# Kernel optimization log

Measured on AMD Instinct MI355X. Metric: run time of the kernel, lower is better.

Reference implementation:

```python
import jax, jax.numpy as jnp
import numpy as np

NB, NQ, NLINKS = 524288, 7, 8


def _cross_matrix(v):
    # v: [..., 3] -> skew-symmetric [..., 3, 3]
    z = jnp.zeros_like(v[..., 0])
    v1, v2, v3 = v[..., 0], v[..., 1], v[..., 2]
    return jnp.stack([
        jnp.stack([z, -v3, v2], axis=-1),
        jnp.stack([v3, z, -v1], axis=-1),
        jnp.stack([-v2, v1, z], axis=-1),
    ], axis=-2)


def _rodrigues(w, th):
    # w: [..., 3] axis (not necessarily unit), th: [...] angle -> [..., 3, 3]
    w_hat = _cross_matrix(w)
    n = jnp.linalg.norm(w, axis=-1)
    a = (jnp.sin(n * th) / n)[..., None, None]
    b = ((1.0 - jnp.cos(n * th)) / (n * n))[..., None, None]
    I = jnp.eye(3, dtype=w.dtype)
    return I + a * w_hat + b * (w_hat @ w_hat)


def _rpy_to_R(rpy):
    # rpy: [n, 3] -> [n, 3, 3]; R = Rz(yaw) @ Ry(pitch) @ Rx(roll)
    n = rpy.shape[0]
    ex = jnp.broadcast_to(jnp.array([1.0, 0.0, 0.0], rpy.dtype), (n, 3))
    ey = jnp.broadcast_to(jnp.array([0.0, 1.0, 0.0], rpy.dtype), (n, 3))
    ez = jnp.broadcast_to(jnp.array([0.0, 0.0, 1.0], rpy.dtype), (n, 3))
    Rx = _rodrigues(ex, rpy[:, 0])
    Ry = _rodrigues(ey, rpy[:, 1])
    Rz = _rodrigues(ez, rpy[:, 2])
    return Rz @ (Ry @ Rx)


def _hom(R, t):
    # R: [..., 3, 3], t: [..., 3] -> [..., 4, 4]
    top = jnp.concatenate([R, t[..., None]], axis=-1)
    last = jnp.broadcast_to(jnp.array([0.0, 0.0, 0.0, 1.0], R.dtype), top.shape[:-2] + (1, 4))
    return jnp.concatenate([top, last], axis=-2)


def setup_inputs() -> dict:
    key = jax.random.key(0)
    k1, k2, k3, k4, k5 = jax.random.split(key, 5)
    return {
        "q": jax.random.normal(k1, (NB, NQ), dtype=jnp.float32),
        "joint_xyz": jax.random.normal(k2, (NQ, 3), dtype=jnp.float32),
        "joint_rpy": jax.random.normal(k3, (NQ, 3), dtype=jnp.float32),
        "joint_axis": jax.random.normal(k4, (NQ, 3), dtype=jnp.float32),
        "link_xyz": jax.random.normal(k5, (NLINKS, 3), dtype=jnp.float32),
        "idx": 6,
    }


def reference(q, joint_xyz, joint_rpy, joint_axis, link_xyz, idx):
    nb, nq = q.shape
    # Constant per-joint fixed frames [nq, 4, 4]
    T_joints = _hom(_rpy_to_R(joint_rpy), joint_xyz)
    # Constant per-link frames (rpy = 0 => identity rotation path) [nlinks, 4, 4]
    T_links = _hom(_rpy_to_R(jnp.zeros_like(link_xyz)), link_xyz)
    # Per-(batch, joint) joint rotation via Rodrigues: w [nq,3], th [nb,nq] -> [nb,nq,3,3]
    Rq = _rodrigues(joint_axis[None, :, :], q)
    Tq = _hom(Rq, jnp.zeros(Rq.shape[:-2] + (3,), Rq.dtype))  # [nb, nq, 4, 4]
    # Per-joint local transform: fixed frame @ joint rotation
    T = T_joints[None, :, :, :] @ Tq  # [nb, nq, 4, 4]
    # Sequential chain over joints (nq is small and fixed)
    T_world = T[:, 0]
    for j in range(1, nq):
        T_world = T_world @ T[:, j]
    return T_world @ T_links[idx][None, :, :]  # [nb, 4, 4]
```

## Files before the change

kernel.cpp:

```cpp
#include <hip/hip_runtime.h>

#define FK_NQ 7
#define FK_BLOCK 256


__device__ __forceinline__ void qmul(const float* a, const float* b, float* r)
{
    r[0] = a[0]*b[0] - a[1]*b[1] - a[2]*b[2] - a[3]*b[3];
    r[1] = a[0]*b[1] + a[1]*b[0] + a[2]*b[3] - a[3]*b[2];
    r[2] = a[0]*b[2] - a[1]*b[3] + a[2]*b[0] + a[3]*b[1];
    r[3] = a[0]*b[3] + a[1]*b[2] - a[2]*b[1] + a[3]*b[0];
}

__global__ __launch_bounds__(FK_BLOCK, 8) void fk_fused(
    const float* __restrict__ q,
    const float* __restrict__ joint_xyz,
    const float* __restrict__ joint_rpy,
    const float* __restrict__ joint_axis,
    const float* __restrict__ link_xyz,
    const int*   __restrict__ idxp,
    float* __restrict__ out,
    unsigned nb)
{
    __shared__ float4 c4[22];
    __shared__ float4 so[FK_BLOCK * 5];

    const int tid = threadIdx.x;
    const unsigned bbase = blockIdx.x * FK_BLOCK;
    const unsigned b = bbase + tid;
    const bool valid = (b < nb);

    float th[FK_NQ];
    if (valid) {
        const float* qp = q + b * FK_NQ;
        #pragma unroll
        for (int j = 0; j < FK_NQ; ++j) th[j] = qp[j];
    }

    if (tid < FK_NQ) {
        const int j = tid;
        float rr = joint_rpy[j*3+0], pp = joint_rpy[j*3+1], yy = joint_rpy[j*3+2];
        float sr, cr, sp2, cp2, sy, cy;
        __sincosf(0.5f*rr, &sr, &cr);
        __sincosf(0.5f*pp, &sp2, &cp2);
        __sincosf(0.5f*yy, &sy, &cy);
        float qx[4] = {cr, sr, 0.f, 0.f};
        float qy[4] = {cp2, 0.f, sp2, 0.f};
        float qz[4] = {cy, 0.f, 0.f, sy};
        float tmp[4], qj[4];
        qmul(qy, qx, tmp);
        qmul(qz, tmp, qj);

        float w0 = joint_axis[j*3+0], w1 = joint_axis[j*3+1], w2 = joint_axis[j*3+2];
        float n  = sqrtf(w0*w0 + w1*w1 + w2*w2);
        float ninv = 1.0f/n;
        float qu[4] = {0.f, w0*ninv, w1*ninv, w2*ninv};
        float qjw[4];
        qmul(qj, qu, qjw);

        c4[j*3+0] = make_float4(qj[0],  qj[1],  qj[2],  qj[3]);
        c4[j*3+1] = make_float4(qjw[0], qjw[1], qjw[2], qjw[3]);
        c4[j*3+2] = make_float4(joint_xyz[j*3+0], joint_xyz[j*3+1],
                                joint_xyz[j*3+2], 0.5f*n);
    } else if (tid == FK_NQ) {
        const int ix = idxp[0];
        c4[21] = make_float4(link_xyz[ix*3+0], link_xyz[ix*3+1],
                             link_xyz[ix*3+2], 0.0f);
    }
    __syncthreads();

    if (valid) {
        float4 j0q = c4[0], j0w = c4[1], j0t = c4[2];
        float sv, cv;
        __sincosf(j0t.w * th[0], &sv, &cv);
        float Qw = cv*j0q.x + sv*j0w.x;
        float Qx = cv*j0q.y + sv*j0w.y;
        float Qy = cv*j0q.z + sv*j0w.z;
        float Qz = cv*j0q.w + sv*j0w.w;
        float tx = j0t.x, ty = j0t.y, tz = j0t.z;

        #pragma unroll
        for (int j = 1; j < FK_NQ; ++j) {
            float4 jq = c4[j*3+0], jw = c4[j*3+1], jt = c4[j*3+2];
            float s, c;
            __sincosf(jt.w * th[j], &s, &c);
            float vx = jt.x, vy = jt.y, vz = jt.z;
            float c1x = Qy*vz - Qz*vy;
            float c1y = Qz*vx - Qx*vz;
            float c1z = Qx*vy - Qy*vx;
            float c2x = Qw*c1x + (Qy*c1z - Qz*c1y);
            float c2y = Qw*c1y + (Qz*c1x - Qx*c1z);
            float c2z = Qw*c1z + (Qx*c1y - Qy*c1x);
            tx += vx + 2.0f*c2x;
            ty += vy + 2.0f*c2y;
            tz += vz + 2.0f*c2z;
            float sw = c*jq.x + s*jw.x;
            float sx = c*jq.y + s*jw.y;
            float sy = c*jq.z + s*jw.z;
            float sz = c*jq.w + s*jw.w;
            float nw = Qw*sw - Qx*sx - Qy*sy - Qz*sz;
            float nx = Qw*sx + Qx*sw + Qy*sz - Qz*sy;
            float ny = Qw*sy - Qx*sz + Qy*sw + Qz*sx;
            float nz = Qw*sz + Qx*sy - Qy*sx + Qz*sw;
            Qw = nw; Qx = nx; Qy = ny; Qz = nz;
        }

        float xx = Qx*Qx, yy = Qy*Qy, zz = Qz*Qz;
        float xy = Qx*Qy, xz = Qx*Qz, yz = Qy*Qz;
        float wx = Qw*Qx, wy = Qw*Qy, wz = Qw*Qz;
        float M00 = 1.0f - 2.0f*(yy+zz);
        float M01 = 2.0f*(xy - wz);
        float M02 = 2.0f*(xz + wy);
        float M10 = 2.0f*(xy + wz);
        float M11 = 1.0f - 2.0f*(xx+zz);
        float M12 = 2.0f*(yz - wx);
        float M20 = 2.0f*(xz - wy);
        float M21 = 2.0f*(yz + wx);
        float M22 = 1.0f - 2.0f*(xx+yy);

        float4 lp = c4[21];
        so[tid*5+0] = make_float4(M00, M01, M02, M00*lp.x + M01*lp.y + M02*lp.z + tx);
        so[tid*5+1] = make_float4(M10, M11, M12, M10*lp.x + M11*lp.y + M12*lp.z + ty);
        so[tid*5+2] = make_float4(M20, M21, M22, M20*lp.x + M21*lp.y + M22*lp.z + tz);
        so[tid*5+3] = make_float4(0.0f, 0.0f, 0.0f, 1.0f);
    }
    __syncthreads();

    if (bbase + FK_BLOCK <= nb) {
        float4* o = (float4*)out + (size_t)bbase * 4u;
        #pragma unroll
        for (int k = 0; k < 4; ++k) {
            unsigned w = k*FK_BLOCK + tid;
            o[w] = so[(w >> 2)*5 + (w & 3)];
        }
    } else if (valid) {
        float4* o = (float4*)(out + (size_t)b * 16u);
        #pragma unroll
        for (int r = 0; r < 4; ++r) o[r] = so[tid*5 + r];
    }
}

extern "C" void kernel_launch(void* const* d_in, const int* in_sizes, int n_in,
                              void* d_out, int out_size, void* d_ws, size_t ws_size,
                              hipStream_t stream) {
    const float* q          = (const float*)d_in[0];
    const float* joint_xyz  = (const float*)d_in[1];
    const float* joint_rpy  = (const float*)d_in[2];
    const float* joint_axis = (const float*)d_in[3];
    const float* link_xyz   = (const float*)d_in[4];
    const int*   idxp       = (const int*)d_in[5];
    float* out = (float*)d_out;

    const unsigned nb = (unsigned)(in_sizes[0] / FK_NQ);
    const int grid = (int)((nb + FK_BLOCK - 1) / FK_BLOCK);

    fk_fused<<<grid, FK_BLOCK, 0, stream>>>(q, joint_xyz, joint_rpy, joint_axis,
                                            link_xyz, idxp, out, nb);
}
```

Measured before the change: 17.18 us.

## Convert to persistent grid-stride kernel with prefetched q and double-buffered staging

Caps the grid at a fixed number of blocks, and each block loops over chunks of the batch. Each iteration prefetches the next chunk's joint angles while computing the current one, and staging alternates between two shared buffers. The per-joint constant setup is then paid once per block rather than once per chunk. The cost is fewer resident waves, doubled shared memory and a dropped occupancy hint in the launch bounds, which may reduce latency hiding on this memory-bound kernel.

```diff
diff --git a/kernel.cpp b/kernel.cpp
--- a/kernel.cpp
+++ b/kernel.cpp
@@ -2,6 +2,7 @@
 
 #define FK_NQ 7
 #define FK_BLOCK 256
+#define MAX_GRID 768
 
 
 __device__ __forceinline__ void qmul(const float* a, const float* b, float* r)
@@ -12,7 +13,7 @@
     r[3] = a[0]*b[3] + a[1]*b[2] - a[2]*b[1] + a[3]*b[0];
 }
 
-__global__ __launch_bounds__(FK_BLOCK, 8) void fk_fused(
+__global__ __launch_bounds__(FK_BLOCK) void fk_fused(
     const float* __restrict__ q,
     const float* __restrict__ joint_xyz,
     const float* __restrict__ joint_rpy,
@@ -23,19 +24,10 @@
     unsigned nb)
 {
     __shared__ float4 c4[22];
-    __shared__ float4 so[FK_BLOCK * 5];
+    __shared__ float4 so[2][FK_BLOCK * 5];
 
     const int tid = threadIdx.x;
-    const unsigned bbase = blockIdx.x * FK_BLOCK;
-    const unsigned b = bbase + tid;
-    const bool valid = (b < nb);
-
-    float th[FK_NQ];
-    if (valid) {
-        const float* qp = q + b * FK_NQ;
-        #pragma unroll
-        for (int j = 0; j < FK_NQ; ++j) th[j] = qp[j];
-    }
+    const unsigned nchunks = (nb + FK_BLOCK - 1) / FK_BLOCK;
 
     if (tid < FK_NQ) {
         const int j = tid;
@@ -67,76 +59,115 @@
         c4[21] = make_float4(link_xyz[ix*3+0], link_xyz[ix*3+1],
                              link_xyz[ix*3+2], 0.0f);
     }
+
+    unsigned c = blockIdx.x;
+    float th[FK_NQ];
+    {
+        const unsigned b = c * FK_BLOCK + tid;
+        if (b < nb) {
+            const float* qp = q + (size_t)b * FK_NQ;
+            #pragma unroll
+            for (int j = 0; j < FK_NQ; ++j) th[j] = qp[j];
+        } else {
+            #pragma unroll
+            for (int j = 0; j < FK_NQ; ++j) th[j] = 0.0f;
+        }
+    }
+
     __syncthreads();
 
-    if (valid) {
-        float4 j0q = c4[0], j0w = c4[1], j0t = c4[2];
-        float sv, cv;
-        __sincosf(j0t.w * th[0], &sv, &cv);
-        float Qw = cv*j0q.x + sv*j0w.x;
-        float Qx = cv*j0q.y + sv*j0w.y;
-        float Qy = cv*j0q.z + sv*j0w.z;
-        float Qz = cv*j0q.w + sv*j0w.w;
-        float tx = j0t.x, ty = j0t.y, tz = j0t.z;
+    int buf = 0;
+    const float4 lp = c4[21];
+
+    for (; c < nchunks; c += gridDim.x) {
+        const unsigned cn = c + gridDim.x;
+        float thn[FK_NQ];
+        #pragma unroll
+        for (int j = 0; j < FK_NQ; ++j) thn[j] = 0.0f;
+        if (cn < nchunks) {
+            const unsigned bn = cn * FK_BLOCK + tid;
+            if (bn < nb) {
+                const float* qp = q + (size_t)bn * FK_NQ;
+                #pragma unroll
+                for (int j = 0; j < FK_NQ; ++j) thn[j] = qp[j];
+            }
+        }
+
+        const unsigned bbase = c * FK_BLOCK;
+        const unsigned b = bbase + tid;
+        if (b < nb) {
+            float sv[FK_NQ], cv[FK_NQ];
+            #pragma unroll
+            for (int j = 0; j < FK_NQ; ++j)
+                __sincosf(c4[j*3+2].w * th[j], &sv[j], &cv[j]);
+
+            float4 j0q = c4[0], j0w = c4[1], j0t = c4[2];
+            float Qw = cv[0]*j0q.x + sv[0]*j0w.x;
+            float Qx = cv[0]*j0q.y + sv[0]*j0w.y;
+            float Qy = cv[0]*j0q.z + sv[0]*j0w.z;
+            float Qz = cv[0]*j0q.w + sv[0]*j0w.w;
+            float tx = j0t.x, ty = j0t.y, tz = j0t.z;
+
+            #pragma unroll
+            for (int j = 1; j < FK_NQ; ++j) {
+                float4 jq = c4[j*3+0], jw = c4[j*3+1], jt = c4[j*3+2];
+                float vx = jt.x, vy = jt.y, vz = jt.z;
+                float c1x = Qy*vz - Qz*vy;
+                float c1y = Qz*vx - Qx*vz;
+                float c1z = Qx*vy - Qy*vx;
+                float c2x = Qw*c1x + (Qy*c1z - Qz*c1y);
+                float c2y = Qw*c1y + (Qz*c1x - Qx*c1z);
+                float c2z = Qw*c1z + (Qx*c1y - Qy*c1x);
+                tx += vx + 2.0f*c2x;
+                ty += vy + 2.0f*c2y;
+                tz += vz + 2.0f*c2z;
+                float sw = cv[j]*jq.x + sv[j]*jw.x;
+                float sx = cv[j]*jq.y + sv[j]*jw.y;
+                float sy2 = cv[j]*jq.z + sv[j]*jw.z;
+                float sz = cv[j]*jq.w + sv[j]*jw.w;
+                float nw = Qw*sw - Qx*sx - Qy*sy2 - Qz*sz;
+                float nx = Qw*sx + Qx*sw + Qy*sz - Qz*sy2;
+                float ny = Qw*sy2 - Qx*sz + Qy*sw + Qz*sx;
+                float nz = Qw*sz + Qx*sy2 - Qy*sx + Qz*sw;
+                Qw = nw; Qx = nx; Qy = ny; Qz = nz;
+            }
+
+            float xx = Qx*Qx, yy = Qy*Qy, zz = Qz*Qz;
+            float xy = Qx*Qy, xz = Qx*Qz, yz = Qy*Qz;
+            float wx = Qw*Qx, wy = Qw*Qy, wz = Qw*Qz;
+            float M00 = 1.0f - 2.0f*(yy+zz);
+            float M01 = 2.0f*(xy - wz);
+            float M02 = 2.0f*(xz + wy);
+            float M10 = 2.0f*(xy + wz);
+            float M11 = 1.0f - 2.0f*(xx+zz);
+            float M12 = 2.0f*(yz - wx);
+            float M20 = 2.0f*(xz - wy);
+            float M21 = 2.0f*(yz + wx);
+            float M22 = 1.0f - 2.0f*(xx+yy);
+
+            so[buf][tid*5+0] = make_float4(M00, M01, M02, M00*lp.x + M01*lp.y + M02*lp.z + tx);
+            so[buf][tid*5+1] = make_float4(M10, M11, M12, M10*lp.x + M11*lp.y + M12*lp.z + ty);
+            so[buf][tid*5+2] = make_float4(M20, M21, M22, M20*lp.x + M21*lp.y + M22*lp.z + tz);
+            so[buf][tid*5+3] = make_float4(0.0f, 0.0f, 0.0f, 1.0f);
+        }
+        __syncthreads();
+
+        if (bbase + FK_BLOCK <= nb) {
+            float4* o = (float4*)out + (size_t)bbase * 4u;
+            #pragma unroll
+            for (int k = 0; k < 4; ++k) {
+                unsigned w = k*FK_BLOCK + tid;
+                o[w] = so[buf][(w >> 2)*5 + (w & 3)];
+            }
+        } else if (b < nb) {
+            float4* o = (float4*)(out + (size_t)b * 16u);
+            #pragma unroll
+            for (int r = 0; r < 4; ++r) o[r] = so[buf][tid*5 + r];
+        }
 
         #pragma unroll
-        for (int j = 1; j < FK_NQ; ++j) {
-            float4 jq = c4[j*3+0], jw = c4[j*3+1], jt = c4[j*3+2];
-            float s, c;
-            __sincosf(jt.w * th[j], &s, &c);
-            float vx = jt.x, vy = jt.y, vz = jt.z;
-            float c1x = Qy*vz - Qz*vy;
-            float c1y = Qz*vx - Qx*vz;
-            float c1z = Qx*vy - Qy*vx;
-            float c2x = Qw*c1x + (Qy*c1z - Qz*c1y);
-            float c2y = Qw*c1y + (Qz*c1x - Qx*c1z);
-            float c2z = Qw*c1z + (Qx*c1y - Qy*c1x);
-            tx += vx + 2.0f*c2x;
-            ty += vy + 2.0f*c2y;
-            tz += vz + 2.0f*c2z;
-            float sw = c*jq.x + s*jw.x;
-            float sx = c*jq.y + s*jw.y;
-            float sy = c*jq.z + s*jw.z;
-            float sz = c*jq.w + s*jw.w;
-            float nw = Qw*sw - Qx*sx - Qy*sy - Qz*sz;
-            float nx = Qw*sx + Qx*sw + Qy*sz - Qz*sy;
-            float ny = Qw*sy - Qx*sz + Qy*sw + Qz*sx;
-            float nz = Qw*sz + Qx*sy - Qy*sx + Qz*sw;
-            Qw = nw; Qx = nx; Qy = ny; Qz = nz;
-        }
-
-        float xx = Qx*Qx, yy = Qy*Qy, zz = Qz*Qz;
-        float xy = Qx*Qy, xz = Qx*Qz, yz = Qy*Qz;
-        float wx = Qw*Qx, wy = Qw*Qy, wz = Qw*Qz;
-        float M00 = 1.0f - 2.0f*(yy+zz);
-        float M01 = 2.0f*(xy - wz);
-        float M02 = 2.0f*(xz + wy);
-        float M10 = 2.0f*(xy + wz);
-        float M11 = 1.0f - 2.0f*(xx+zz);
-        float M12 = 2.0f*(yz - wx);
-        float M20 = 2.0f*(xz - wy);
-        float M21 = 2.0f*(yz + wx);
-        float M22 = 1.0f - 2.0f*(xx+yy);
-
-        float4 lp = c4[21];
-        so[tid*5+0] = make_float4(M00, M01, M02, M00*lp.x + M01*lp.y + M02*lp.z + tx);
-        so[tid*5+1] = make_float4(M10, M11, M12, M10*lp.x + M11*lp.y + M12*lp.z + ty);
-        so[tid*5+2] = make_float4(M20, M21, M22, M20*lp.x + M21*lp.y + M22*lp.z + tz);
-        so[tid*5+3] = make_float4(0.0f, 0.0f, 0.0f, 1.0f);
-    }
-    __syncthreads();
-
-    if (bbase + FK_BLOCK <= nb) {
-        float4* o = (float4*)out + (size_t)bbase * 4u;
-        #pragma unroll
-        for (int k = 0; k < 4; ++k) {
-            unsigned w = k*FK_BLOCK + tid;
-            o[w] = so[(w >> 2)*5 + (w & 3)];
-        }
-    } else if (valid) {
-        float4* o = (float4*)(out + (size_t)b * 16u);
-        #pragma unroll
-        for (int r = 0; r < 4; ++r) o[r] = so[tid*5 + r];
+        for (int j = 0; j < FK_NQ; ++j) th[j] = thn[j];
+        buf ^= 1;
     }
 }
 
@@ -152,7 +183,8 @@
     float* out = (float*)d_out;
 
     const unsigned nb = (unsigned)(in_sizes[0] / FK_NQ);
-    const int grid = (int)((nb + FK_BLOCK - 1) / FK_BLOCK);
+    const unsigned nchunks = (nb + FK_BLOCK - 1) / FK_BLOCK;
+    const unsigned grid = nchunks < MAX_GRID ? nchunks : MAX_GRID;
 
     fk_fused<<<grid, FK_BLOCK, 0, stream>>>(q, joint_xyz, joint_rpy, joint_axis,
                                             link_xyz, idxp, out, nb);
```

New measurement: 17.55 us. 2.2% more time.
